# Performance work log

Measured on AMD Instinct MI355X. Metric: run time of the kernel, lower is better.

The kernel has to match this reference:

```python
import jax, jax.numpy as jnp
import numpy as np

D = 128

def setup_inputs() -> dict:
    key = jax.random.key(0)
    k1, k2, k3, k4, k5, k6, k7 = jax.random.split(key, 7)
    B, L = 2048, 200
    target = jax.random.normal(k1, (B, D), dtype=jnp.float32)
    item_seq = jax.random.normal(k2, (B, L, D), dtype=jnp.float32)
    seq_len = jax.random.randint(k3, (B,), 0, 200, dtype=jnp.int64 if jax.config.jax_enable_x64 else jnp.int32)
    # MLP params: Linear(4D -> 2D), Linear(2D -> 1), PyTorch-style init scale
    s1 = 1.0 / np.sqrt(4 * D)
    s2 = 1.0 / np.sqrt(2 * D)
    W1 = jax.random.uniform(k4, (4 * D, 2 * D), minval=-s1, maxval=s1, dtype=jnp.float32)
    b1 = jax.random.uniform(k5, (2 * D,), minval=-s1, maxval=s1, dtype=jnp.float32)
    W2 = jax.random.uniform(k6, (2 * D, 1), minval=-s2, maxval=s2, dtype=jnp.float32)
    b2 = jax.random.uniform(k7, (1,), minval=-s2, maxval=s2, dtype=jnp.float32)
    return {"target": target, "item_seq": item_seq, "seq_len": seq_len,
            "W1": W1, "b1": b1, "W2": W2, "b2": b2}

def reference(target, item_seq, seq_len, W1, b1, W2, b2):
    B, L, Dd = item_seq.shape
    t = target[:, None, :]                              # B 1 D (broadcast over L)
    tgt = jnp.broadcast_to(t, (B, L, Dd))
    sub = item_seq - tgt
    dot = item_seq * tgt
    mlp_in = jnp.concatenate([tgt, item_seq, sub, dot], axis=-1)   # B L 4D
    h = jax.nn.relu(jnp.einsum('blf,fh->blh', mlp_in, W1) + b1)    # B L 2D
    score = jnp.einsum('blh,ho->blo', h, W2) + b2                  # B L 1
    mask = (jnp.arange(L)[None, :] < seq_len[:, None]).astype(item_seq.dtype)  # B L
    weighted = score * item_seq * mask[:, :, None]                 # B L D
    return jnp.sum(weighted, axis=1)                               # B D
```

## Files before the change

kernel.cpp:

```cpp
#include <hip/hip_runtime.h>
#include <hip/hip_bf16.h>

typedef short short8 __attribute__((ext_vector_type(8)));
typedef float f32x4 __attribute__((ext_vector_type(4)));

#define XS 136

static __device__ inline short f2bf(float f) {
    unsigned u = __float_as_uint(f);
    unsigned r = (u + 0x7fffu + ((u >> 16) & 1u)) >> 16;
    return (short)r;
}
static __device__ inline float bf2f(short s) {
    return __uint_as_float(((unsigned)(unsigned short)s) << 16);
}

__global__ void prep(const float* __restrict__ W1, short* __restrict__ Wbc,
                     short* __restrict__ Wd) {
    int idx = blockIdx.x * 256 + threadIdx.x;
    int half = idx >> 15;
    int i = idx & 32767;
    int j = i & 7;
    int l = (i >> 3) & 63;
    int s = (i >> 9) & 3;
    int t = i >> 11;
    int k = s * 32 + ((l >> 4) << 3) + j;
    int n = t * 16 + (l & 15);
    if (half == 0) Wbc[i] = f2bf(W1[(128 + k) * 256 + n] + W1[(256 + k) * 256 + n]);
    else           Wd[i]  = f2bf(W1[(384 + k) * 256 + n]);
}

__global__ void compute_u(const float* __restrict__ target, const float* __restrict__ W1,
                          const float* __restrict__ b1, float* __restrict__ U) {
    const int b8 = blockIdx.x;
    const int tid = threadIdx.x;
    __shared__ float tl[1024];
#pragma unroll
    for (int k = 0; k < 4; k++) tl[k * 256 + tid] = target[b8 * 1024 + k * 256 + tid];
    __syncthreads();
    float acc[8] = {0.f, 0.f, 0.f, 0.f, 0.f, 0.f, 0.f, 0.f};
#pragma unroll 8
    for (int d = 0; d < 128; ++d) {
        float wud = W1[d * 256 + tid] - W1[(256 + d) * 256 + tid];
#pragma unroll
        for (int r = 0; r < 8; r++) acc[r] += tl[r * 128 + d] * wud;
    }
    float bj = b1[tid];
#pragma unroll
    for (int r = 0; r < 8; r++) U[(b8 * 8 + r) * 256 + tid] = acc[r] + bj;
}

__launch_bounds__(256, 2)
__global__ void din_main(const float* __restrict__ target, const float* __restrict__ item_seq,
                         const int* __restrict__ seq_len, const float* __restrict__ W2,
                         const float* __restrict__ b2p, const short* __restrict__ Wbc,
                         const short* __restrict__ Wd, const float* __restrict__ U,
                         float* __restrict__ out) {
    const int b = blockIdx.x;
    const int tid = threadIdx.x;
    const int lane = tid & 63;
    const int w = tid >> 6;
    const int col = lane & 15;
    const int q = lane >> 4;

    const int slen = seq_len[b];
    const int nt = (slen + 15) >> 4;

    __shared__ __attribute__((aligned(16))) short Xl[2][16 * XS];
    __shared__ __attribute__((aligned(16))) float tsh[128];
    __shared__ float u_s[256];
    __shared__ float w2_s[256];
    __shared__ __attribute__((aligned(16))) float scoreP[16][4];
    __shared__ float out_s[128];

    const int r = tid >> 4;
    const int c = (tid & 15) << 3;

    float4 v0, v1;
    {
        const float4* src = (const float4*)(item_seq + (((size_t)b * 200 + r) * 128 + c));
        v0 = src[0]; v1 = src[1];
    }

    if (tid < 128) tsh[tid] = target[b * 128 + tid];
    u_s[tid] = U[b * 256 + tid];
    w2_s[tid] = W2[tid];
    const float b2 = b2p[0];
    __syncthreads();

    short8 bfrag[4][4];
#pragma unroll
    for (int s = 0; s < 4; s++) {
        const float4* tp = (const float4*)(tsh + s * 32 + q * 8);
        float4 ta = tp[0], tb = tp[1];
        float tk[8] = {ta.x, ta.y, ta.z, ta.w, tb.x, tb.y, tb.z, tb.w};
#pragma unroll
        for (int i = 0; i < 4; i++) {
            size_t off = ((size_t)((w * 4 + i) * 4 + s) * 64 + lane) * 8;
            short8 bc = *(const short8*)(Wbc + off);
            short8 dd = *(const short8*)(Wd + off);
            short8 e;
#pragma unroll
            for (int j = 0; j < 8; j++) e[j] = f2bf(bf2f(bc[j]) + tk[j] * bf2f(dd[j]));
            bfrag[i][s] = e;
        }
    }

    float u_c[4], w2c[4];
#pragma unroll
    for (int i = 0; i < 4; i++) {
        int j = (w * 4 + i) * 16 + col;
        u_c[i] = u_s[j];
        w2c[i] = w2_s[j];
    }

    const int d = tid & 127;
    const int g = tid >> 7;
    float out_val = 0.f;
    f32x4 acc[4];

    for (int mt = 0; mt < nt; ++mt) {
        const int l0 = mt * 16;
        short* xb = Xl[mt & 1];

        {
            float v[8] = {v0.x, v0.y, v0.z, v0.w, v1.x, v1.y, v1.z, v1.w};
            short8 p;
#pragma unroll
            for (int j = 0; j < 8; j++) p[j] = f2bf(v[j]);
            *(short8*)(xb + r * XS + c) = p;
        }
        __syncthreads();

        if (mt + 1 < nt) {
            int lr = l0 + 16 + r;
            if (lr > 199) lr = 199;
            const float4* src = (const float4*)(item_seq + (((size_t)b * 200 + lr) * 128 + c));
            v0 = src[0]; v1 = src[1];
        }

#pragma unroll
        for (int i = 0; i < 4; i++) acc[i] = (f32x4){0.f, 0.f, 0.f, 0.f};
        const short* arow = xb + col * XS + q * 8;
#pragma unroll
        for (int s = 0; s < 4; s++) {
            short8 af = *(const short8*)(arow + s * 32);
#pragma unroll
            for (int i = 0; i < 4; i++)
                acc[i] = __builtin_amdgcn_mfma_f32_16x16x32_bf16(af, bfrag[i][s], acc[i], 0, 0, 0);
        }

        float sv[4];
#pragma unroll
        for (int rg = 0; rg < 4; rg++) {
            float s0 = 0.f;
#pragma unroll
            for (int i = 0; i < 4; i++) {
                float h = acc[i][rg] + u_c[i];
                h = h > 0.f ? h : 0.f;
                s0 += h * w2c[i];
            }
            sv[rg] = s0;
        }
#pragma unroll
        for (int off = 1; off < 16; off <<= 1) {
#pragma unroll
            for (int rg = 0; rg < 4; rg++) sv[rg] += __shfl_xor(sv[rg], off, 64);
        }
        if (col == 0) {
#pragma unroll
            for (int rg = 0; rg < 4; rg++) scoreP[q * 4 + rg][w] = sv[rg];
        }
        __syncthreads();

#pragma unroll
        for (int mm = 0; mm < 8; mm++) {
            int m = g * 8 + mm;
            int l = l0 + m;
            float4 sp = *(const float4*)&scoreP[m][0];
            float s = (sp.x + sp.y) + (sp.z + sp.w) + b2;
            s = (l < slen) ? s : 0.f;
            out_val += s * bf2f(xb[m * XS + d]);
        }
    }

    __syncthreads();
    if (g == 1) out_s[d] = out_val;
    __syncthreads();
    if (g == 0) out[b * 128 + d] = out_val + out_s[d];
}

extern "C" void kernel_launch(void* const* d_in, const int* in_sizes, int n_in,
                              void* d_out, int out_size, void* d_ws, size_t ws_size,
                              hipStream_t stream) {
    const float* target   = (const float*)d_in[0];
    const float* item_seq = (const float*)d_in[1];
    const int*   seq_len  = (const int*)d_in[2];
    const float* W1       = (const float*)d_in[3];
    const float* b1       = (const float*)d_in[4];
    const float* W2       = (const float*)d_in[5];
    const float* b2       = (const float*)d_in[6];
    float* out = (float*)d_out;

    char* ws = (char*)d_ws;
    short* Wbc = (short*)ws;
    short* Wd  = (short*)(ws + 65536);
    float* U   = (float*)(ws + 131072);

    prep<<<256, 256, 0, stream>>>(W1, Wbc, Wd);
    compute_u<<<256, 256, 0, stream>>>(target, W1, b1, U);
    din_main<<<2048, 256, 0, stream>>>(target, item_seq, seq_len, W2, b2, Wbc, Wd, U, out);
}
```

Before: 312.8 us.

## Pipeline score accumulation one tile behind, merge prep kernels, use packed bf16 converts

The main loop now removes the second barrier per tile. The weighted-sum accumulation for tile mt-1 runs after tile mt's MFMA, using a 4-deep X buffer and double-buffered score partials. The two preprocessing kernels are merged into one launch. Bias U is folded into the MFMA accumulator init, and bf16 conversion uses the packed v_cvt_pk_bf16_f32 instruction. This cuts barriers, a launch and conversion ALU work, at the cost of more LDS per block, which may affect occupancy.

```diff
diff --git a/kernel.cpp b/kernel.cpp
--- a/kernel.cpp
+++ b/kernel.cpp
@@ -14,27 +14,32 @@
 static __device__ inline float bf2f(short s) {
     return __uint_as_float(((unsigned)(unsigned short)s) << 16);
 }
-
-__global__ void prep(const float* __restrict__ W1, short* __restrict__ Wbc,
-                     short* __restrict__ Wd) {
-    int idx = blockIdx.x * 256 + threadIdx.x;
-    int half = idx >> 15;
-    int i = idx & 32767;
-    int j = i & 7;
-    int l = (i >> 3) & 63;
-    int s = (i >> 9) & 3;
-    int t = i >> 11;
-    int k = s * 32 + ((l >> 4) << 3) + j;
-    int n = t * 16 + (l & 15);
-    if (half == 0) Wbc[i] = f2bf(W1[(128 + k) * 256 + n] + W1[(256 + k) * 256 + n]);
-    else           Wd[i]  = f2bf(W1[(384 + k) * 256 + n]);
-}
-
-__global__ void compute_u(const float* __restrict__ target, const float* __restrict__ W1,
-                          const float* __restrict__ b1, float* __restrict__ U) {
+static __device__ inline unsigned cvtpk(float lo, float hi) {
+    unsigned r;
+    asm("v_cvt_pk_bf16_f32 %0, %1, %2" : "=v"(r) : "v"(lo), "v"(hi));
+    return r;
+}
+
+__global__ void precompute(const float* __restrict__ W1, const float* __restrict__ b1,
+                           const float* __restrict__ target, short* __restrict__ Wbc,
+                           short* __restrict__ Wd, float* __restrict__ U) {
+    __shared__ float tl[1024];
+    const int tid = threadIdx.x;
+    if (blockIdx.x >= 256) {
+        int idx = (blockIdx.x - 256) * 256 + tid;
+        int half = idx >> 15;
+        int i = idx & 32767;
+        int j = i & 7;
+        int l = (i >> 3) & 63;
+        int s = (i >> 9) & 3;
+        int t = i >> 11;
+        int k = s * 32 + ((l >> 4) << 3) + j;
+        int n = t * 16 + (l & 15);
+        if (half == 0) Wbc[i] = f2bf(W1[(128 + k) * 256 + n] + W1[(256 + k) * 256 + n]);
+        else           Wd[i]  = f2bf(W1[(384 + k) * 256 + n]);
+        return;
+    }
     const int b8 = blockIdx.x;
-    const int tid = threadIdx.x;
-    __shared__ float tl[1024];
 #pragma unroll
     for (int k = 0; k < 4; k++) tl[k * 256 + tid] = target[b8 * 1024 + k * 256 + tid];
     __syncthreads();
@@ -66,11 +71,11 @@
     const int slen = seq_len[b];
     const int nt = (slen + 15) >> 4;
 
-    __shared__ __attribute__((aligned(16))) short Xl[2][16 * XS];
+    __shared__ __attribute__((aligned(16))) short Xl[4][16 * XS];
     __shared__ __attribute__((aligned(16))) float tsh[128];
     __shared__ float u_s[256];
     __shared__ float w2_s[256];
-    __shared__ __attribute__((aligned(16))) float scoreP[16][4];
+    __shared__ __attribute__((aligned(16))) float scoreP[2][16][4];
     __shared__ float out_s[128];
 
     const int r = tid >> 4;
@@ -99,10 +104,20 @@
             size_t off = ((size_t)((w * 4 + i) * 4 + s) * 64 + lane) * 8;
             short8 bc = *(const short8*)(Wbc + off);
             short8 dd = *(const short8*)(Wd + off);
-            short8 e;
-#pragma unroll
-            for (int j = 0; j < 8; j++) e[j] = f2bf(bf2f(bc[j]) + tk[j] * bf2f(dd[j]));
-            bfrag[i][s] = e;
+            float f0 = fmaf(tk[0], bf2f(dd[0]), bf2f(bc[0]));
+            float f1 = fmaf(tk[1], bf2f(dd[1]), bf2f(bc[1]));
+            float f2 = fmaf(tk[2], bf2f(dd[2]), bf2f(bc[2]));
+            float f3 = fmaf(tk[3], bf2f(dd[3]), bf2f(bc[3]));
+            float f4 = fmaf(tk[4], bf2f(dd[4]), bf2f(bc[4]));
+            float f5 = fmaf(tk[5], bf2f(dd[5]), bf2f(bc[5]));
+            float f6 = fmaf(tk[6], bf2f(dd[6]), bf2f(bc[6]));
+            float f7 = fmaf(tk[7], bf2f(dd[7]), bf2f(bc[7]));
+            uint4 pe;
+            pe.x = cvtpk(f0, f1);
+            pe.y = cvtpk(f2, f3);
+            pe.z = cvtpk(f4, f5);
+            pe.w = cvtpk(f6, f7);
+            bfrag[i][s] = *(short8*)&pe;
         }
     }
 
@@ -117,30 +132,45 @@
     const int d = tid & 127;
     const int g = tid >> 7;
     float out_val = 0.f;
-    f32x4 acc[4];
+
+    auto accum_tile = [&](int pt) {
+        const short* xp = Xl[pt & 3];
+        const int l0p = pt * 16;
+        const float4* spb = (const float4*)scoreP[pt & 1];
+#pragma unroll
+        for (int mm = 0; mm < 8; mm++) {
+            int m = g * 8 + mm;
+            int l = l0p + m;
+            float4 sp = spb[m];
+            float s = (sp.x + sp.y) + (sp.z + sp.w) + b2;
+            s = (l < slen) ? s : 0.f;
+            out_val = fmaf(s, bf2f(xp[m * XS + d]), out_val);
+        }
+    };
 
     for (int mt = 0; mt < nt; ++mt) {
-        const int l0 = mt * 16;
-        short* xb = Xl[mt & 1];
+        short* xb = Xl[mt & 3];
 
         {
-            float v[8] = {v0.x, v0.y, v0.z, v0.w, v1.x, v1.y, v1.z, v1.w};
-            short8 p;
-#pragma unroll
-            for (int j = 0; j < 8; j++) p[j] = f2bf(v[j]);
-            *(short8*)(xb + r * XS + c) = p;
+            uint4 pk;
+            pk.x = cvtpk(v0.x, v0.y);
+            pk.y = cvtpk(v0.z, v0.w);
+            pk.z = cvtpk(v1.x, v1.y);
+            pk.w = cvtpk(v1.z, v1.w);
+            *(uint4*)(xb + r * XS + c) = pk;
         }
         __syncthreads();
 
         if (mt + 1 < nt) {
-            int lr = l0 + 16 + r;
+            int lr = (mt + 1) * 16 + r;
             if (lr > 199) lr = 199;
             const float4* src = (const float4*)(item_seq + (((size_t)b * 200 + lr) * 128 + c));
             v0 = src[0]; v1 = src[1];
         }
 
-#pragma unroll
-        for (int i = 0; i < 4; i++) acc[i] = (f32x4){0.f, 0.f, 0.f, 0.f};
+        f32x4 acc[4];
+#pragma unroll
+        for (int i = 0; i < 4; i++) acc[i] = (f32x4){u_c[i], u_c[i], u_c[i], u_c[i]};
         const short* arow = xb + col * XS + q * 8;
 #pragma unroll
         for (int s = 0; s < 4; s++) {
@@ -156,9 +186,9 @@
             float s0 = 0.f;
 #pragma unroll
             for (int i = 0; i < 4; i++) {
-                float h = acc[i][rg] + u_c[i];
+                float h = acc[i][rg];
                 h = h > 0.f ? h : 0.f;
-                s0 += h * w2c[i];
+                s0 = fmaf(h, w2c[i], s0);
             }
             sv[rg] = s0;
         }
@@ -169,19 +199,15 @@
         }
         if (col == 0) {
 #pragma unroll
-            for (int rg = 0; rg < 4; rg++) scoreP[q * 4 + rg][w] = sv[rg];
-        }
+            for (int rg = 0; rg < 4; rg++) scoreP[mt & 1][q * 4 + rg][w] = sv[rg];
+        }
+
+        if (mt > 0) accum_tile(mt - 1);
+    }
+
+    if (nt > 0) {
         __syncthreads();
-
-#pragma unroll
-        for (int mm = 0; mm < 8; mm++) {
-            int m = g * 8 + mm;
-            int l = l0 + m;
-            float4 sp = *(const float4*)&scoreP[m][0];
-            float s = (sp.x + sp.y) + (sp.z + sp.w) + b2;
-            s = (l < slen) ? s : 0.f;
-            out_val += s * bf2f(xb[m * XS + d]);
-        }
+        accum_tile(nt - 1);
     }
 
     __syncthreads();
@@ -207,7 +233,6 @@
     short* Wd  = (short*)(ws + 65536);
     float* U   = (float*)(ws + 131072);
 
-    prep<<<256, 256, 0, stream>>>(W1, Wbc, Wd);
-    compute_u<<<256, 256, 0, stream>>>(target, W1, b1, U);
+    precompute<<<512, 256, 0, stream>>>(W1, b1, target, Wbc, Wd, U);
     din_main<<<2048, 256, 0, stream>>>(target, item_seq, seq_len, W2, b2, Wbc, Wd, U, out);
 }
```

Result: faster. 300.9 us (-3.8%).
